# Optimization experiments

Hardware: AMD Instinct MI355X
Metric: run time of the kernel (lower is better)

The kernel has to match this reference:

```python
import jax, jax.numpy as jnp
import numpy as np


def dct_mat(N, dtype=jnp.float32):
    # Orthonormal DCT-II matrix M: X = M @ x matches scipy dct(norm='ortho').
    n = jnp.arange(N, dtype=dtype)
    k = n[:, None]
    M = jnp.cos(jnp.pi * (2.0 * n[None, :] + 1.0) * k / (2.0 * N)) * jnp.sqrt(2.0 / N)
    M = M.at[0].multiply(1.0 / jnp.sqrt(2.0))
    return M


def setup_inputs() -> dict:
    key = jax.random.key(0)
    k1, k2, k3 = jax.random.split(key, 3)
    B, C, H, W = 8, 128, 200, 480  # H = 5*W/12 required by the slice/reshape logic
    x = jax.random.normal(k1, (B, C, H, W), dtype=jnp.float32)
    # nn.Linear(input_dim, input_dim//4, bias=False) weight: [C//4, C]
    w1 = jax.random.normal(k2, (C // 4, C), dtype=jnp.float32) * (1.0 / np.sqrt(C))
    # nn.Linear(input_dim//4, input_dim, bias=False) weight: [C, C//4]
    w2 = jax.random.normal(k3, (C, C // 4), dtype=jnp.float32) * (1.0 / np.sqrt(C // 4))
    return {"x": x, "w1": w1, "w2": w2}


def reference(x, w1, w2):
    LOW_W, HIGH_W = 0.6, 0.4
    B, C, H, W = x.shape
    D = dct_mat(W, x.dtype)
    # DCT-II (ortho) along the last (width) axis
    x_dct = jnp.einsum('bchn,kn->bchk', x, D)
    sp1, sp2 = W // 2, W // 4  # split points from x_dct.shape[-1]
    hs = H - sp2               # high-freq start index (uses height!)
    low = x_dct[:, :, :sp1, :sp1]                     # [B,C,min(H,sp1),sp1]
    high = x_dct[:, :, hs:, hs:].reshape(B, C, low.shape[2], low.shape[3])
    bal = LOW_W * low + HIGH_W * high
    # IDCT (DCT-III, ortho) along the last axis of the balanced spectrum
    D2 = dct_mat(low.shape[3], x.dtype)
    x_bal = jnp.einsum('bchk,kn->bchn', bal, D2)
    gap = jnp.mean(x_bal, axis=(2, 3))                # [B,C]
    att = jax.nn.sigmoid((gap @ w1.T) @ w2.T)         # SE-style channel gate
    return x * att[:, :, None, None]
```

## Files before the change

### kernel.cpp

```cpp
#include <hip/hip_runtime.h>
#include <math.h>


namespace {

constexpr int Hh    = 200;
constexpr int Ww    = 480;
constexpr int PLANE = Hh * Ww;
constexpr int NBC   = 8 * 128;
constexpr int ROW4  = Ww / 4;

__global__ __launch_bounds__(256, 4) void gap_kernel(const float* __restrict__ x,
                                                     float2* __restrict__ pq) {
    __shared__ __align__(16) float Wt[4][Ww];
    __shared__ float redp[4], redq[4];
    const int t = threadIdx.x;

    const float s   = 0.06454972243679028f;
    const float c2a = (float)(M_PI / 960.0);
    for (int n = t; n < Ww; n += 256) {
        int tn = 2 * n + 1;
        Wt[0][n] = s * (__cosf((float)((tn *  80) % 1920) * c2a) +
                        __cosf((float)((tn * 320) % 1920) * c2a));
        Wt[1][n] = s * (__cosf((float)((tn * 160) % 1920) * c2a) +
                        __cosf((float)((tn * 400) % 1920) * c2a));
        Wt[2][n] = s *  __cosf((float)((tn * 240) % 1920) * c2a);
        Wt[3][n] = 0.f;
    }
    __syncthreads();

    const int wave = t >> 6, lane = t & 63;
    const int bc = blockIdx.x >> 1, part = blockIdx.x & 1;
    const int r0 = part * 100;
    const float4* xp = (const float4*)(x + (size_t)bc * PLANE);
    const bool has2 = lane < (ROW4 - 64);
    const float4 z4 = {0.f, 0.f, 0.f, 0.f};

    float p = 0.f, q = 0.f;
    for (int tile = 0; tile < 6; tile++) {
        const int hb = r0 + tile * 16 + wave * 4;
        #pragma unroll
        for (int rr = 0; rr < 4; rr++) {
            const int h = hb + rr;
            const float4* row = xp + h * ROW4;
            float4 v  = row[lane];
            float4 v2 = has2 ? row[lane + 64] : z4;
            const int cls = (h < 80) ? 3 : (h - 80) % 3;
            const float4* wrow = (const float4*)Wt[cls];
            float4 wv  = wrow[lane];
            float4 wv2 = has2 ? wrow[lane + 64] : z4;
            p += (v.x + v.y) + (v.z + v.w) + (v2.x + v2.y) + (v2.z + v2.w);
            q += v.x * wv.x + v.y * wv.y + v.z * wv.z + v.w * wv.w
               + v2.x * wv2.x + v2.y * wv2.y + v2.z * wv2.z + v2.w * wv2.w;
        }
    }
    {
        const int h = r0 + 96 + wave;
        const float4* row = xp + h * ROW4;
        float4 v  = row[lane];
        float4 v2 = has2 ? row[lane + 64] : z4;
        const int cls = (h < 80) ? 3 : (h - 80) % 3;
        const float4* wrow = (const float4*)Wt[cls];
        float4 wv  = wrow[lane];
        float4 wv2 = has2 ? wrow[lane + 64] : z4;
        p += (v.x + v.y) + (v.z + v.w) + (v2.x + v2.y) + (v2.z + v2.w);
        q += v.x * wv.x + v.y * wv.y + v.z * wv.z + v.w * wv.w
           + v2.x * wv2.x + v2.y * wv2.y + v2.z * wv2.z + v2.w * wv2.w;
    }

    #pragma unroll
    for (int o = 32; o > 0; o >>= 1) {
        p += __shfl_down(p, o);
        q += __shfl_down(q, o);
    }
    if (lane == 0) { redp[wave] = p; redq[wave] = q; }
    __syncthreads();
    if (t == 0) {
        float P = (redp[0] + redp[1]) + (redp[2] + redp[3]);
        float Q = (redq[0] + redq[1]) + (redq[2] + redq[3]);
        pq[blockIdx.x] = make_float2(P, Q);
    }
}

__global__ __launch_bounds__(256) void att_kernel(const float2* __restrict__ pq,
                                                  const float* __restrict__ w1,
                                                  const float* __restrict__ w2,
                                                  float* __restrict__ att) {
    __shared__ float g[128];
    __shared__ float t1[32];
    const int b = blockIdx.x, t = threadIdx.x;
    if (t < 128) {
        float2 a0 = pq[(b * 128 + t) * 2 + 0];
        float2 a1 = pq[(b * 128 + t) * 2 + 1];
        float P = a0.x + a1.x, Q = a0.y + a1.y;
        g[t] = (0.02738612787525831f * P + 0.4f * Q) * 3.227486121839514e-4f;
    }
    __syncthreads();
    if (t < 32) {
        float acc = 0.f;
        #pragma unroll
        for (int c = 0; c < 128; c++) acc += g[c] * w1[t * 128 + c];
        t1[t] = acc;
    }
    __syncthreads();
    if (t < 128) {
        float acc = 0.f;
        #pragma unroll
        for (int j = 0; j < 32; j++) acc += t1[j] * w2[t * 32 + j];
        att[b * 128 + t] = 1.f / (1.f + __expf(-acc));
    }
}

__global__ __launch_bounds__(256) void scale_kernel(const float* __restrict__ x,
                                                    const float* __restrict__ att,
                                                    float* __restrict__ out) {
    const int bc = (NBC - 1) - (int)blockIdx.x;
    const float a = att[bc];
    const float4* __restrict__ xp = (const float4*)(x   + (size_t)bc * PLANE);
    float4* __restrict__       op = (float4*)      (out + (size_t)bc * PLANE);
    const int start = blockIdx.y * 6000;
    const int end   = start + 6000;
    int i = start + (int)threadIdx.x;
    for (; i + 768 < end; i += 1024) {
        float4 v0 = xp[i], v1 = xp[i + 256], v2 = xp[i + 512], v3 = xp[i + 768];
        v0.x *= a; v0.y *= a; v0.z *= a; v0.w *= a;
        v1.x *= a; v1.y *= a; v1.z *= a; v1.w *= a;
        v2.x *= a; v2.y *= a; v2.z *= a; v2.w *= a;
        v3.x *= a; v3.y *= a; v3.z *= a; v3.w *= a;
        op[i] = v0; op[i + 256] = v1; op[i + 512] = v2; op[i + 768] = v3;
    }
    for (; i < end; i += 256) {
        float4 v = xp[i];
        v.x *= a; v.y *= a; v.z *= a; v.w *= a;
        op[i] = v;
    }
}

}

extern "C" void kernel_launch(void* const* d_in, const int* in_sizes, int n_in,
                              void* d_out, int out_size, void* d_ws, size_t ws_size,
                              hipStream_t stream) {
    const float* x  = (const float*)d_in[0];
    const float* w1 = (const float*)d_in[1];
    const float* w2 = (const float*)d_in[2];
    float* out = (float*)d_out;
    float2* pq = (float2*)d_ws;
    float* att = (float*)d_ws + 4096;

    gap_kernel<<<NBC * 2, 256, 0, stream>>>(x, pq);
    att_kernel<<<8, 256, 0, stream>>>(pq, w1, w2, att);
    scale_kernel<<<dim3(NBC, 4), 256, 0, stream>>>(x, att, out);
}
```

Baseline: 716.3 us.

## Pipeline per-batch GAP and scale passes in fused launches with nontemporal IO

New measurement: 688.9 us. 3.8% less time.

```diff
diff --git a/kernel.cpp b/kernel.cpp
--- a/kernel.cpp
+++ b/kernel.cpp
@@ -7,41 +7,68 @@
 constexpr int Hh    = 200;
 constexpr int Ww    = 480;
 constexpr int PLANE = Hh * Ww;
-constexpr int NBC   = 8 * 128;
+constexpr int CH    = 128;
 constexpr int ROW4  = Ww / 4;
 
-__global__ __launch_bounds__(256, 4) void gap_kernel(const float* __restrict__ x,
-                                                     float2* __restrict__ pq) {
-    __shared__ __align__(16) float Wt[4][Ww];
-    __shared__ float redp[4], redq[4];
+typedef float f32x4 __attribute__((ext_vector_type(4)));
+
+__global__ __launch_bounds__(256, 4) void pipe_kernel(
+    const float* __restrict__ x,
+    const float* __restrict__ w1,
+    const float* __restrict__ w2,
+    float2* __restrict__ pq,
+    float* __restrict__ out,
+    const int gap_batch,
+    const int scale_batch) {
+
     const int t = threadIdx.x;
+    const int gap_nb = (gap_batch >= 0) ? 2 * CH : 0;
 
-    const float s   = 0.06454972243679028f;
-    const float c2a = (float)(M_PI / 960.0);
-    for (int n = t; n < Ww; n += 256) {
-        int tn = 2 * n + 1;
-        Wt[0][n] = s * (__cosf((float)((tn *  80) % 1920) * c2a) +
-                        __cosf((float)((tn * 320) % 1920) * c2a));
-        Wt[1][n] = s * (__cosf((float)((tn * 160) % 1920) * c2a) +
-                        __cosf((float)((tn * 400) % 1920) * c2a));
-        Wt[2][n] = s *  __cosf((float)((tn * 240) % 1920) * c2a);
-        Wt[3][n] = 0.f;
-    }
-    __syncthreads();
+    if ((int)blockIdx.x < gap_nb) {
+        __shared__ __align__(16) float Wt[4][Ww];
+        __shared__ float redp[4], redq[4];
 
-    const int wave = t >> 6, lane = t & 63;
-    const int bc = blockIdx.x >> 1, part = blockIdx.x & 1;
-    const int r0 = part * 100;
-    const float4* xp = (const float4*)(x + (size_t)bc * PLANE);
-    const bool has2 = lane < (ROW4 - 64);
-    const float4 z4 = {0.f, 0.f, 0.f, 0.f};
+        const float s   = 0.06454972243679028f;
+        const float c2a = (float)(M_PI / 960.0);
+        for (int n = t; n < Ww; n += 256) {
+            int tn = 2 * n + 1;
+            Wt[0][n] = s * (__cosf((float)((tn *  80) % 1920) * c2a) +
+                            __cosf((float)((tn * 320) % 1920) * c2a));
+            Wt[1][n] = s * (__cosf((float)((tn * 160) % 1920) * c2a) +
+                            __cosf((float)((tn * 400) % 1920) * c2a));
+            Wt[2][n] = s *  __cosf((float)((tn * 240) % 1920) * c2a);
+            Wt[3][n] = 0.f;
+        }
+        __syncthreads();
 
-    float p = 0.f, q = 0.f;
-    for (int tile = 0; tile < 6; tile++) {
-        const int hb = r0 + tile * 16 + wave * 4;
-        #pragma unroll
-        for (int rr = 0; rr < 4; rr++) {
-            const int h = hb + rr;
+        const int wave = t >> 6, lane = t & 63;
+        const int c = blockIdx.x >> 1, part = blockIdx.x & 1;
+        const int bc = gap_batch * CH + c;
+        const int r0 = part * 100;
+        const float4* xp = (const float4*)(x + (size_t)bc * PLANE);
+        const bool has2 = lane < (ROW4 - 64);
+        const float4 z4 = {0.f, 0.f, 0.f, 0.f};
+
+        float p = 0.f, q = 0.f;
+        for (int tile = 0; tile < 6; tile++) {
+            const int hb = r0 + tile * 16 + wave * 4;
+            #pragma unroll
+            for (int rr = 0; rr < 4; rr++) {
+                const int h = hb + rr;
+                const float4* row = xp + h * ROW4;
+                float4 v  = row[lane];
+                float4 v2 = has2 ? row[lane + 64] : z4;
+                const int cls = (h < 80) ? 3 : (h - 80) % 3;
+                const float4* wrow = (const float4*)Wt[cls];
+                float4 wv  = wrow[lane];
+                float4 wv2 = has2 ? wrow[lane + 64] : z4;
+                p += (v.x + v.y) + (v.z + v.w) + (v2.x + v2.y) + (v2.z + v2.w);
+                q += v.x * wv.x + v.y * wv.y + v.z * wv.z + v.w * wv.w
+                   + v2.x * wv2.x + v2.y * wv2.y + v2.z * wv2.z + v2.w * wv2.w;
+            }
+        }
+        {
+            const int h = r0 + 96 + wave;
             const float4* row = xp + h * ROW4;
             float4 v  = row[lane];
             float4 v2 = has2 ? row[lane + 64] : z4;
@@ -53,86 +80,71 @@
             q += v.x * wv.x + v.y * wv.y + v.z * wv.z + v.w * wv.w
                + v2.x * wv2.x + v2.y * wv2.y + v2.z * wv2.z + v2.w * wv2.w;
         }
-    }
-    {
-        const int h = r0 + 96 + wave;
-        const float4* row = xp + h * ROW4;
-        float4 v  = row[lane];
-        float4 v2 = has2 ? row[lane + 64] : z4;
-        const int cls = (h < 80) ? 3 : (h - 80) % 3;
-        const float4* wrow = (const float4*)Wt[cls];
-        float4 wv  = wrow[lane];
-        float4 wv2 = has2 ? wrow[lane + 64] : z4;
-        p += (v.x + v.y) + (v.z + v.w) + (v2.x + v2.y) + (v2.z + v2.w);
-        q += v.x * wv.x + v.y * wv.y + v.z * wv.z + v.w * wv.w
-           + v2.x * wv2.x + v2.y * wv2.y + v2.z * wv2.z + v2.w * wv2.w;
-    }
 
-    #pragma unroll
-    for (int o = 32; o > 0; o >>= 1) {
-        p += __shfl_down(p, o);
-        q += __shfl_down(q, o);
-    }
-    if (lane == 0) { redp[wave] = p; redq[wave] = q; }
-    __syncthreads();
-    if (t == 0) {
-        float P = (redp[0] + redp[1]) + (redp[2] + redp[3]);
-        float Q = (redq[0] + redq[1]) + (redq[2] + redq[3]);
-        pq[blockIdx.x] = make_float2(P, Q);
-    }
-}
+        #pragma unroll
+        for (int o = 32; o > 0; o >>= 1) {
+            p += __shfl_down(p, o);
+            q += __shfl_down(q, o);
+        }
+        if (lane == 0) { redp[wave] = p; redq[wave] = q; }
+        __syncthreads();
+        if (t == 0) {
+            float P = (redp[0] + redp[1]) + (redp[2] + redp[3]);
+            float Q = (redq[0] + redq[1]) + (redq[2] + redq[3]);
+            pq[bc * 2 + part] = make_float2(P, Q);
+        }
+    } else {
+        const int sb = (int)blockIdx.x - gap_nb;
+        const int c = sb >> 2, chunk = sb & 3;
+        const int bc = scale_batch * CH + c;
 
-__global__ __launch_bounds__(256) void att_kernel(const float2* __restrict__ pq,
-                                                  const float* __restrict__ w1,
-                                                  const float* __restrict__ w2,
-                                                  float* __restrict__ att) {
-    __shared__ float g[128];
-    __shared__ float t1[32];
-    const int b = blockIdx.x, t = threadIdx.x;
-    if (t < 128) {
-        float2 a0 = pq[(b * 128 + t) * 2 + 0];
-        float2 a1 = pq[(b * 128 + t) * 2 + 1];
-        float P = a0.x + a1.x, Q = a0.y + a1.y;
-        g[t] = (0.02738612787525831f * P + 0.4f * Q) * 3.227486121839514e-4f;
-    }
-    __syncthreads();
-    if (t < 32) {
-        float acc = 0.f;
-        #pragma unroll
-        for (int c = 0; c < 128; c++) acc += g[c] * w1[t * 128 + c];
-        t1[t] = acc;
-    }
-    __syncthreads();
-    if (t < 128) {
-        float acc = 0.f;
-        #pragma unroll
-        for (int j = 0; j < 32; j++) acc += t1[j] * w2[t * 32 + j];
-        att[b * 128 + t] = 1.f / (1.f + __expf(-acc));
-    }
-}
+        __shared__ float g[CH];
+        __shared__ float t1s[32];
+        __shared__ float ash;
+        if (t < CH) {
+            float2 a0 = pq[(scale_batch * CH + t) * 2 + 0];
+            float2 a1 = pq[(scale_batch * CH + t) * 2 + 1];
+            float P = a0.x + a1.x, Q = a0.y + a1.y;
+            g[t] = (0.02738612787525831f * P + 0.4f * Q) * 3.227486121839514e-4f;
+        }
+        __syncthreads();
+        if (t < 32) {
+            float acc = 0.f;
+            #pragma unroll
+            for (int cc = 0; cc < CH; cc++) acc += g[cc] * w1[t * CH + cc];
+            t1s[t] = acc;
+        }
+        __syncthreads();
+        if (t == 0) {
+            float acc = 0.f;
+            #pragma unroll
+            for (int j = 0; j < 32; j++) acc += t1s[j] * w2[c * 32 + j];
+            ash = 1.f / (1.f + __expf(-acc));
+        }
+        __syncthreads();
+        const float a = ash;
 
-__global__ __launch_bounds__(256) void scale_kernel(const float* __restrict__ x,
-                                                    const float* __restrict__ att,
-                                                    float* __restrict__ out) {
-    const int bc = (NBC - 1) - (int)blockIdx.x;
-    const float a = att[bc];
-    const float4* __restrict__ xp = (const float4*)(x   + (size_t)bc * PLANE);
-    float4* __restrict__       op = (float4*)      (out + (size_t)bc * PLANE);
-    const int start = blockIdx.y * 6000;
-    const int end   = start + 6000;
-    int i = start + (int)threadIdx.x;
-    for (; i + 768 < end; i += 1024) {
-        float4 v0 = xp[i], v1 = xp[i + 256], v2 = xp[i + 512], v3 = xp[i + 768];
-        v0.x *= a; v0.y *= a; v0.z *= a; v0.w *= a;
-        v1.x *= a; v1.y *= a; v1.z *= a; v1.w *= a;
-        v2.x *= a; v2.y *= a; v2.z *= a; v2.w *= a;
-        v3.x *= a; v3.y *= a; v3.z *= a; v3.w *= a;
-        op[i] = v0; op[i + 256] = v1; op[i + 512] = v2; op[i + 768] = v3;
-    }
-    for (; i < end; i += 256) {
-        float4 v = xp[i];
-        v.x *= a; v.y *= a; v.z *= a; v.w *= a;
-        op[i] = v;
+        const f32x4* __restrict__ xv = (const f32x4*)(x   + (size_t)bc * PLANE);
+        f32x4* __restrict__       ov = (f32x4*)      (out + (size_t)bc * PLANE);
+        const int start = chunk * 6000;
+        const int end   = start + 6000;
+        int i = start + t;
+        for (; i + 768 < end; i += 1024) {
+            f32x4 v0 = __builtin_nontemporal_load(xv + i);
+            f32x4 v1 = __builtin_nontemporal_load(xv + i + 256);
+            f32x4 v2 = __builtin_nontemporal_load(xv + i + 512);
+            f32x4 v3 = __builtin_nontemporal_load(xv + i + 768);
+            v0 *= a; v1 *= a; v2 *= a; v3 *= a;
+            __builtin_nontemporal_store(v0, ov + i);
+            __builtin_nontemporal_store(v1, ov + i + 256);
+            __builtin_nontemporal_store(v2, ov + i + 512);
+            __builtin_nontemporal_store(v3, ov + i + 768);
+        }
+        for (; i < end; i += 256) {
+            f32x4 v = __builtin_nontemporal_load(xv + i);
+            v *= a;
+            __builtin_nontemporal_store(v, ov + i);
+        }
     }
 }
 
@@ -146,9 +158,9 @@
     const float* w2 = (const float*)d_in[2];
     float* out = (float*)d_out;
     float2* pq = (float2*)d_ws;
-    float* att = (float*)d_ws + 4096;
 
-    gap_kernel<<<NBC * 2, 256, 0, stream>>>(x, pq);
-    att_kernel<<<8, 256, 0, stream>>>(pq, w1, w2, att);
-    scale_kernel<<<dim3(NBC, 4), 256, 0, stream>>>(x, att, out);
+    pipe_kernel<<<256, 256, 0, stream>>>(x, w1, w2, pq, out, 0, -1);
+    for (int b = 1; b < 8; b++)
+        pipe_kernel<<<768, 256, 0, stream>>>(x, w1, w2, pq, out, b, b - 1);
+    pipe_kernel<<<512, 256, 0, stream>>>(x, w1, w2, pq, out, -1, 7);
 }
```
